# Kernel tuning notes

Hardware: AMD Instinct MI355X
Metric: run time of the kernel (lower is better)

Reference implementation:

```python
import jax, jax.numpy as jnp
import numpy as np

B, S, D, K, DF, H, DFF = 2, 512, 512, 8, 64, 8, 2048
DH = D // H  # d_head = 64
CS = D // K  # chunk_size = 64


def layer_norm(x, g, b, eps=1e-5):
    m = x.mean(-1, keepdims=True)
    v = ((x - m) ** 2).mean(-1, keepdims=True)
    return (x - m) / jnp.sqrt(v + eps) * g + b


def matexp_taylor(M, terms=6):
    # exp(M) ~= I + M + M^2/2! + ... (6 terms), batched over leading dims
    I = jnp.broadcast_to(jnp.eye(M.shape[-1], dtype=M.dtype), M.shape)
    res, P = I, I
    for n in range(1, terms + 1):
        P = jnp.matmul(P, M) / n
        res = res + P
    return res


def setup_inputs() -> dict:
    key = jax.random.key(0)
    ks = jax.random.split(key, 24)
    w = lambda k, shape, s=0.02: (jax.random.normal(k, shape, jnp.float32) * s)
    return {
        'x': jax.random.normal(ks[0], (B, S, D), jnp.float32),
        'u': jax.random.normal(ks[1], (B, S, DF), jnp.float32),
        'Wq': w(ks[2], (D, D)), 'bq': jnp.zeros((D,), jnp.float32),
        'Wk': w(ks[3], (D, D)), 'bk': jnp.zeros((D,), jnp.float32),
        'Wv': w(ks[4], (D, D)), 'bv': jnp.zeros((D,), jnp.float32),
        'Wo': w(ks[5], (D, D)), 'bo': jnp.zeros((D,), jnp.float32),
        'Wfp': w(ks[6], (DF, D)), 'bfp': jnp.zeros((D,), jnp.float32),
        'Wfo': w(ks[7], (D, DF)), 'bfo': jnp.zeros((DF,), jnp.float32),
        'Wc1': w(ks[8], (D, DFF)), 'bc1': jnp.zeros((DFF,), jnp.float32),
        'g_ln': jnp.ones((DFF,), jnp.float32), 'b_ln': jnp.zeros((DFF,), jnp.float32),
        # small scale keeps the Lie elements O(1) so the Taylor matexp is well-behaved
        'Wc2': w(ks[9], (DFF, D * K * K), 0.001), 'bc2': jnp.zeros((D * K * K,), jnp.float32),
    }


def reference(x, u, Wq, bq, Wk, bk, Wv, bv, Wo, bo, Wfp, bfp, Wfo, bfo,
              Wc1, bc1, g_ln, b_ln, Wc2, bc2):
    b, s, d = x.shape
    # --- ConnectionNetwork: A[b,s,d,k,k] ---
    h = jax.nn.gelu(x @ Wc1 + bc1, approximate=False)
    h = layer_norm(h, g_ln, b_ln)
    A = (h @ Wc2 + bc2).reshape(b, s, d, K, K)
    # --- ParallelTransport: lie[b,i,j] = sum_d (x_i - x_j)_d * A[j,d]  ---
    # (split into x_i.A_j and x_j.A_j terms to avoid [b,s,s,d,k,k] intermediate)
    lie = jnp.einsum('bid,bjdkl->bijkl', x, A) - jnp.einsum('bjd,bjdkl->bjkl', x, A)[:, None]
    Gamma = matexp_taylor(-lie)  # [b,s,s,k,k], Gamma[b,i,j] transports j->i
    # --- standard multi-head attention on x (eval mode, no dropout, no mask) ---
    q = (x @ Wq + bq).reshape(b, s, H, DH).transpose(0, 2, 1, 3)
    k_ = (x @ Wk + bk).reshape(b, s, H, DH).transpose(0, 2, 1, 3)
    v = (x @ Wv + bv).reshape(b, s, H, DH).transpose(0, 2, 1, 3)
    scores = jnp.einsum('bhid,bhjd->bhij', q, k_) / jnp.sqrt(jnp.float32(DH))
    attn = jax.nn.softmax(scores, axis=-1)
    ctx = jnp.einsum('bhij,bhjd->bhid', attn, v).transpose(0, 2, 1, 3).reshape(b, s, d)
    x_out = x + ctx @ Wo + bo
    # --- fiber transport: u_i += sum_j attn_avg[i,j] * Gamma[i,j] @ u_chunks[j] ---
    u_proj = u @ Wfp + bfp                      # [b,s,D]
    u_chunks = u_proj.reshape(b, s, K, CS)      # [b,s,k,cs]
    attn_avg = attn.mean(axis=1)                # [b,s,s]
    weighted = Gamma * attn_avg[..., None, None]
    u_t = jnp.einsum('bijkl,bjlc->bikc', weighted, u_chunks).reshape(b, s, d)
    u_out = u + u_t @ Wfo + bfo
    return (x_out, u_out)
```

## Files before the change

### kernel.cpp

```cpp
#include <hip/hip_runtime.h>
#include <math.h>

#define BB 2
#define SS 512
#define DD 512
#define HH 8
#define DFF 2048

typedef __attribute__((ext_vector_type(8))) short bf16x8;
typedef __attribute__((ext_vector_type(4))) float f32x4;

__device__ __forceinline__ float gelu_exact(float v) {
    return 0.5f * v * (1.0f + erff(v * 0.70710678118654752f));
}
__device__ __forceinline__ unsigned short f2bf(float f) {
    unsigned u = __float_as_uint(f);
    u += 0x7FFF + ((u >> 16) & 1);
    return (unsigned short)(u >> 16);
}
__device__ __forceinline__ float bf2f(unsigned short s) {
    return __uint_as_float(((unsigned)s) << 16);
}
__device__ __forceinline__ void gload16(const void* g, void* l) {
    __builtin_amdgcn_global_load_lds((const __attribute__((address_space(1))) void*)g,
                                     (__attribute__((address_space(3))) void*)l, 16, 0, 0);
}

template<int NT, int EPI, int SK = 1>
__global__ __launch_bounds__(256)
void mgemm_k(const unsigned short* __restrict__ A, const unsigned short* __restrict__ B,
             const float* __restrict__ bias, const float* __restrict__ resid,
             float* __restrict__ Cf, unsigned short* __restrict__ Cb,
             int K, int lda, int ldb, int ldc, int batchH,
             long aSB, long aSH, long bSB, long bSH, long cSB, long cSH,
             float scale)
{
    __shared__ unsigned short As[128][32];
    __shared__ unsigned short Bs[NT][32];
    const int tid = threadIdx.x;
    const int wave = tid >> 6, lane = tid & 63;
    const int z = blockIdx.z;
    const int zb = z / batchH, zh = z % batchH;
    const unsigned short* Ab = A + (long)zb * aSB + (long)zh * aSH;
    const unsigned short* Bb = B + (long)zb * bSB + (long)zh * bSH;
    const int chunk = (SK > 1) ? ((int)blockIdx.x % SK) : 0;
    const int colb  = (SK > 1) ? ((int)blockIdx.x / SK) : (int)blockIdx.x;
    const int row0 = blockIdx.y * 128, col0 = colb * NT;
    const int wm = wave >> 1, wn = wave & 1;
    const int lm = lane & 15, quad = lane >> 4;
    const int lrow = lane >> 2, lk = (lane & 3) * 8;
    constexpr int NTW = NT / 32;
    f32x4 acc[4][NTW];
    #pragma unroll
    for (int i = 0; i < 4; ++i)
        #pragma unroll
        for (int j = 0; j < NTW; ++j) acc[i][j] = (f32x4)0.f;

    const int kLo = chunk * (K / SK), kHi = kLo + K / SK;
    for (int k0 = kLo; k0 < kHi; k0 += 32) {
        #pragma unroll
        for (int t = 0; t < 2; ++t) {
            const int r = wave * 32 + t * 16;
            gload16(Ab + (long)(row0 + r + lrow) * lda + k0 + lk, &As[r][0]);
        }
        if (NT == 128) {
            #pragma unroll
            for (int t = 0; t < 2; ++t) {
                const int r = wave * 32 + t * 16;
                gload16(Bb + (long)(col0 + r + lrow) * ldb + k0 + lk, &Bs[r][0]);
            }
        } else {
            const int r = wave * 16;
            gload16(Bb + (long)(col0 + r + lrow) * ldb + k0 + lk, &Bs[r][0]);
        }
        __syncthreads();
        bf16x8 af[4], bfr[NTW];
        #pragma unroll
        for (int mt = 0; mt < 4; ++mt)
            af[mt] = *(const bf16x8*)&As[wm * 64 + mt * 16 + lm][quad * 8];
        #pragma unroll
        for (int nt = 0; nt < NTW; ++nt)
            bfr[nt] = *(const bf16x8*)&Bs[wn * (NT / 2) + nt * 16 + lm][quad * 8];
        #pragma unroll
        for (int mt = 0; mt < 4; ++mt)
            #pragma unroll
            for (int nt = 0; nt < NTW; ++nt)
                acc[mt][nt] = __builtin_amdgcn_mfma_f32_16x16x32_bf16(
                    af[mt], bfr[nt], acc[mt][nt], 0, 0, 0);
        __syncthreads();
    }
    float* Cfz = (Cf && EPI != 7) ? Cf + (long)zb * cSB + (long)zh * cSH : Cf;
    unsigned short* Cbz = Cb ? Cb + (long)zb * cSB + (long)zh * cSH : nullptr;
    #pragma unroll
    for (int mt = 0; mt < 4; ++mt) {
        #pragma unroll
        for (int nt = 0; nt < NTW; ++nt) {
            #pragma unroll
            for (int r = 0; r < 4; ++r) {
                const int row = row0 + wm * 64 + mt * 16 + quad * 4 + r;
                const int col = col0 + wn * (NT / 2) + nt * 16 + lm;
                float v = acc[mt][nt][r] * scale;
                if (EPI == 2)      v += bias[(col & 511) * 64 + (col >> 9)];
                else if (EPI == 1 || EPI == 4) v += bias[col];
                else if ((EPI == 3 || EPI == 5 || EPI == 6) && bias) v += bias[col];
                if (EPI == 1) v = gelu_exact(v);
                if (EPI == 4) v += resid[(long)row * ldc + col];
                if (EPI == 0 || EPI == 1 || EPI == 4)
                    Cfz[(long)row * ldc + col] = v;
                else if (EPI == 7)
                    Cf[(long)z * cSB + (long)chunk * cSH + (long)row * ldc + col] = v;
                else if (EPI == 2 || EPI == 3)
                    Cbz[(long)row * ldc + col] = f2bf(v);
                else if (EPI == 5)
                    Cb[(long)(row >> 9) * 262144 + (col >> 6) * 32768 +
                       (col & 63) * 512 + (row & 511)] = f2bf(v);
                else if (EPI == 6)
                    Cb[(long)(row >> 9) * 262144 + (col & 63) * 4096 +
                       (row & 511) * 8 + (col >> 6)] = f2bf(v);
            }
        }
    }
}

__global__ __launch_bounds__(256)
void redqk_k(const float* __restrict__ p, const float* __restrict__ bias,
             unsigned short* __restrict__ out)
{
    const long idx = (long)blockIdx.x * 256 + threadIdx.x;
    const float s = p[idx] + p[idx + 524288] + p[idx + 1048576] + p[idx + 1572864]
                  + bias[idx & 511];
    out[idx] = f2bf(s);
}
__global__ __launch_bounds__(256)
void redv_k(const float* __restrict__ p, const float* __restrict__ bias,
            unsigned short* __restrict__ vT)
{
    const long idx = (long)blockIdx.x * 256 + threadIdx.x;
    const int col = (int)(idx & 511);
    const float s = p[idx] + p[idx + 524288] + p[idx + 1048576] + p[idx + 1572864]
                  + bias[col];
    vT[(idx >> 18) * 262144 + (col >> 6) * 32768 + (col & 63) * 512 +
       ((idx >> 9) & 511)] = f2bf(s);
}
__global__ __launch_bounds__(256)
void redwo_k(const float* __restrict__ p, const float* __restrict__ bias,
             const float* __restrict__ resid, float* __restrict__ out)
{
    const long idx = (long)blockIdx.x * 256 + threadIdx.x;
    out[idx] = resid[idx] + bias[idx & 511]
             + p[idx] + p[idx + 524288] + p[idx + 1048576] + p[idx + 1572864];
}
template<int SK>
__global__ __launch_bounds__(256)
void redzc_k(const float* __restrict__ p, unsigned short* __restrict__ out)
{
    const long idx = (long)blockIdx.x * 256 + threadIdx.x;
    float s = 0.f;
    #pragma unroll
    for (int k = 0; k < SK; ++k) s += p[idx + (long)k * 524288];
    const int b = (int)(idx >> 18), zh = (int)((idx >> 15) & 7);
    const long rem = idx & 32767;
    const int i = (int)(rem >> 6), c = (int)(rem & 63);
    out[(long)b * 262144 + (long)i * 512 + zh * 64 + c] = f2bf(s);
}
__global__ __launch_bounds__(256)
void redu_k(const float* __restrict__ p, const float* __restrict__ bias,
            const float* __restrict__ resid, float* __restrict__ out)
{
    const long idx = (long)blockIdx.x * 256 + threadIdx.x;
    out[idx] = resid[idx] + bias[idx & 63]
             + p[idx] + p[idx + 65536] + p[idx + 131072] + p[idx + 196608];
}

__global__ __launch_bounds__(512, 2)
void fc2_k(const unsigned short* __restrict__ A, const unsigned short* __restrict__ Bm,
           const float* __restrict__ bias, unsigned short* __restrict__ C)
{
    extern __shared__ unsigned short smraw[];
#define SMA(ab, h) (smraw + (((ab) * 2 + (h)) * 8192))
#define SMB(bb, h) (smraw + (32768 + ((bb) * 2 + (h)) * 8192))
    const int tid = threadIdx.x;
    const int wave = tid >> 6, lane = tid & 63;
    const int bid = blockIdx.x;
    const int lin = (bid & 7) * 64 + (bid >> 3);
    const int by = lin & 3, bx = lin >> 2;
    const int row0 = by * 256, col0 = bx * 256;
    const int wm = wave >> 2, wn = wave & 3;
    const int lm = lane & 15, quad = lane >> 4;
    const int axor = lm & 7;
    const int arow = (wm * 64 + lm) * 64;
    const int brow = (wn * 32 + lm) * 64;
    const int ca0 = ((quad) ^ axor) * 8;
    const int ca1 = ((quad + 4) ^ axor) * 8;
    const int srow = wave * 8 + (lane >> 3);
    const int scx = ((lane & 7) ^ ((lane >> 3) & 7)) * 8;
    const int sbrow = ((srow >> 5) << 6) + (srow & 31);
    const unsigned short* AgB = A + (long)(row0 + srow) * 2048 + scx;
    const unsigned short* BgB = Bm + (long)(col0 + sbrow) * 2048 + scx;

    f32x4 acc[8][4];
    #pragma unroll
    for (int i = 0; i < 8; ++i)
        #pragma unroll
        for (int j = 0; j < 4; ++j) acc[i][j] = (f32x4)0.f;
    bf16x8 afr[4][2], b0f[2][2], b1f[2][2];

#define STGA(ab, h, toff) do { \
        const unsigned short* _g = AgB + (toff) * 64 + (h) * (64 * 2048); \
        unsigned short* _d = SMA(ab, h) + wave * 512; \
        gload16(_g, _d); \
        gload16(_g + 128 * 2048, _d + 4096); \
    } while (0)
#define STGB(bb, h, toff) do { \
        const unsigned short* _g = BgB + (toff) * 64 + (h) * (32 * 2048); \
        unsigned short* _d = SMB(bb, h) + wave * 512; \
        gload16(_g, _d); \
        gload16(_g + 128 * 2048, _d + 4096); \
    } while (0)
#define RDA(Hp) do { _Pragma("unroll") for (int _m = 0; _m < 4; ++_m) { \
        afr[_m][0] = *(const bf16x8*)((Hp) + arow + _m * 1024 + ca0); \
        afr[_m][1] = *(const bf16x8*)((Hp) + arow + _m * 1024 + ca1); } } while (0)
#define RDB(bf, Hp) do { _Pragma("unroll") for (int _n = 0; _n < 2; ++_n) { \
        bf[_n][0] = *(const bf16x8*)((Hp) + brow + _n * 1024 + ca0); \
        bf[_n][1] = *(const bf16x8*)((Hp) + brow + _n * 1024 + ca1); } } while (0)
#define MM(QM, QN, bf) do { _Pragma("unroll") for (int _m = 0; _m < 4; ++_m) \
        _Pragma("unroll") for (int _n = 0; _n < 2; ++_n) { \
        acc[(QM)*4+_m][(QN)*2+_n] = __builtin_amdgcn_mfma_f32_16x16x32_bf16( \
            afr[_m][0], bf[_n][0], acc[(QM)*4+_m][(QN)*2+_n], 0, 0, 0); \
        acc[(QM)*4+_m][(QN)*2+_n] = __builtin_amdgcn_mfma_f32_16x16x32_bf16( \
            afr[_m][1], bf[_n][1], acc[(QM)*4+_m][(QN)*2+_n], 0, 0, 0); } } while (0)
#define PH_MID() \
        __builtin_amdgcn_s_barrier(); \
        asm volatile("s_waitcnt lgkmcnt(0)" ::: "memory"); \
        __builtin_amdgcn_sched_barrier(0); \
        __builtin_amdgcn_s_setprio(1)
#define PH_END(VM) \
        __builtin_amdgcn_s_setprio(0); \
        __builtin_amdgcn_sched_barrier(0); \
        asm volatile("s_waitcnt vmcnt(" #VM ")" ::: "memory"); \
        __builtin_amdgcn_sched_barrier(0); \
        __builtin_amdgcn_s_barrier()
#define PH_END_NW() \
        __builtin_amdgcn_s_setprio(0); \
        __builtin_amdgcn_sched_barrier(0); \
        __builtin_amdgcn_s_barrier()

    STGB(0, 0, 0);
    STGB(0, 1, 0);
    STGA(0, 0, 0);
    STGA(0, 1, 0);
    STGB(1, 0, 1);
    STGB(1, 1, 1);
    asm volatile("s_waitcnt vmcnt(6)" ::: "memory");
    __builtin_amdgcn_s_barrier();

    int rA = 0;
    int rB = 0, mB = 1, wB = 2;
    #pragma unroll 1
    for (int t = 0; t < 32; ++t) {
        const int tA = (t + 1 < 32) ? (t + 1) : 31;
        const int tB = (t + 2 < 32) ? (t + 2) : 31;
        const unsigned short* A0p = SMA(rA, 0);
        const unsigned short* A1p = SMA(rA, 1);
        const unsigned short* B0p = SMB(rB, 0);
        const unsigned short* B1p = SMB(rB, 1);
        RDA(A0p); RDB(b0f, B0p);
        STGA(rA ^ 1, 0, tA);
        PH_MID(); MM(0, 0, b0f); PH_END_NW();
        RDB(b1f, B1p);
        STGA(rA ^ 1, 1, tA);
        PH_MID(); MM(0, 1, b1f); PH_END(8);
        RDA(A1p);
        STGB(wB, 0, tB);
        PH_MID(); MM(1, 1, b1f); PH_END_NW();
        STGB(wB, 1, tB);
        PH_MID(); MM(1, 0, b0f); PH_END(6);
        rA ^= 1;
        const int tmp = rB; rB = mB; mB = wB; wB = tmp;
    }
    asm volatile("s_waitcnt vmcnt(0)" ::: "memory");

    const int crow = row0 + wm * 128 + quad * 4;
    const int ccol0 = col0 + wn * 64 + lm;
    #pragma unroll
    for (int ms = 0; ms < 8; ++ms)
        #pragma unroll
        for (int ns = 0; ns < 4; ++ns) {
            const int col = ccol0 + ns * 16;
            const float bv = bias[(col & 511) * 64 + (col >> 9)];
            #pragma unroll
            for (int r = 0; r < 4; ++r) {
                const int row = crow + ms * 16 + r;
                C[(long)row * 32768 + col] = f2bf(acc[ms][ns][r] + bv);
            }
        }
#undef SMA
#undef SMB
#undef STGA
#undef STGB
#undef RDA
#undef RDB
#undef MM
#undef PH_MID
#undef PH_END
#undef PH_END_NW
}

__global__ __launch_bounds__(256)
void liegamma_k(const unsigned short* __restrict__ xb, const unsigned short* __restrict__ At,
                const float* __restrict__ xa, const float* __restrict__ aavg,
                unsigned short* __restrict__ Gw)
{
    __shared__ unsigned short Xs[128][32];
    __shared__ unsigned short Ts[64][32];
    __shared__ float Ml[128][68];
    const int tid = threadIdx.x;
    const int wave = tid >> 6, lane = tid & 63;
    const int b = blockIdx.z, j = blockIdx.y;
    const int i0 = blockIdx.x * 128;
    const int lm = lane & 15, quad = lane >> 4;
    const int lrow = lane >> 2, lk = (lane & 3) * 8;
    const unsigned short* Xb = xb + ((long)b * 512 + i0) * 512;
    const unsigned short* Tb = At + ((long)(b * 512 + j)) * 32768;
    f32x4 acc[2][4];
    #pragma unroll
    for (int i = 0; i < 2; ++i)
        #pragma unroll
        for (int n = 0; n < 4; ++n) acc[i][n] = (f32x4)0.f;

    for (int k0 = 0; k0 < 512; k0 += 32) {
        #pragma unroll
        for (int t = 0; t < 2; ++t) {
            const int r = wave * 32 + t * 16;
            gload16(Xb + (long)(r + lrow) * 512 + k0 + lk, &Xs[r][0]);
        }
        {
            const int r = wave * 16;
            gload16(Tb + (long)(r + lrow) * 512 + k0 + lk, &Ts[r][0]);
        }
        __syncthreads();
        bf16x8 af[2], bfr[4];
        #pragma unroll
        for (int mt = 0; mt < 2; ++mt)
            af[mt] = *(const bf16x8*)&Xs[wave * 32 + mt * 16 + lm][quad * 8];
        #pragma unroll
        for (int nt = 0; nt < 4; ++nt)
            bfr[nt] = *(const bf16x8*)&Ts[nt * 16 + lm][quad * 8];
        #pragma unroll
        for (int mt = 0; mt < 2; ++mt)
            #pragma unroll
            for (int nt = 0; nt < 4; ++nt)
                acc[mt][nt] = __builtin_amdgcn_mfma_f32_16x16x32_bf16(
                    af[mt], bfr[nt], acc[mt][nt], 0, 0, 0);
        __syncthreads();
    }
    const float* xar = xa + ((long)(b * 512 + j)) * 64;
    #pragma unroll
    for (int mt = 0; mt < 2; ++mt)
        #pragma unroll
        for (int nt = 0; nt < 4; ++nt) {
            const float xv = xar[nt * 16 + lm];
            #pragma unroll
            for (int r = 0; r < 4; ++r)
                Ml[wave * 32 + mt * 16 + quad * 4 + r][nt * 16 + lm] = xv - acc[mt][nt][r];
        }
    __syncthreads();
    const int r8 = tid & 7, mg = tid >> 3;
    #pragma unroll 1
    for (int pass = 0; pass < 4; ++pass) {
        const int mi = pass * 32 + mg;
        const f32x4* Mr = (const f32x4*)&Ml[mi][0];
        f32x4 Mreg[16];
        #pragma unroll
        for (int l = 0; l < 16; ++l) Mreg[l] = Mr[l];
        float P[8], res[8];
        #pragma unroll
        for (int c = 0; c < 8; ++c) { const float iv = (c == r8) ? 1.f : 0.f; P[c] = iv; res[c] = iv; }
        #pragma unroll
        for (int n = 1; n <= 6; ++n) {
            float tmp[8] = {0.f,0.f,0.f,0.f,0.f,0.f,0.f,0.f};
            const float invn = 1.f / (float)n;
            #pragma unroll
            for (int l = 0; l < 8; ++l) {
                const f32x4 m0 = Mreg[l * 2], m1 = Mreg[l * 2 + 1];
                const float pl = P[l];
                #pragma unroll
                for (int c = 0; c < 4; ++c) {
                    tmp[c]     = fmaf(pl, m0[c], tmp[c]);
                    tmp[4 + c] = fmaf(pl, m1[c], tmp[4 + c]);
                }
            }
            #pragma unroll
            for (int c = 0; c < 8; ++c) { P[c] = tmp[c] * invn; res[c] += P[c]; }
        }
        const float av = aavg[((long)b * 512 + i0 + mi) * 512 + j];
        bf16x8 o;
        #pragma unroll
        for (int c = 0; c < 8; ++c) o[c] = (short)f2bf(res[c] * av);
        *(bf16x8*)(Gw + ((long)(b * 8 + r8) * 512 + (i0 + mi)) * 4096 + (long)j * 8) = o;
    }
}

__global__ __launch_bounds__(256)
void lnbf_k(const float* __restrict__ h, const float* __restrict__ g,
            const float* __restrict__ b, unsigned short* __restrict__ out)
{
    const long row = blockIdx.x;
    const float* r = h + row * (long)DFF;
    const int tid = threadIdx.x;
    float vals[8];
    float s = 0.f, sq = 0.f;
    #pragma unroll
    for (int e = 0; e < 8; ++e) {
        const float v = r[tid + e * 256];
        vals[e] = v; s += v; sq += v * v;
    }
    __shared__ float rs[256], rq[256];
    rs[tid] = s; rq[tid] = sq; __syncthreads();
    for (int st = 128; st > 0; st >>= 1) {
        if (tid < st) { rs[tid] += rs[tid + st]; rq[tid] += rq[tid + st]; }
        __syncthreads();
    }
    const float mean = rs[0] * (1.f / DFF);
    const float var  = rq[0] * (1.f / DFF) - mean * mean;
    const float inv  = rsqrtf(var + 1e-5f);
    unsigned short* o = out + row * (long)DFF;
    #pragma unroll
    for (int e = 0; e < 8; ++e) {
        const int c = tid + e * 256;
        o[c] = f2bf((vals[e] - mean) * inv * g[c] + b[c]);
    }
}

__global__ __launch_bounds__(256)
void xa_k(const float* __restrict__ x, const unsigned short* __restrict__ At,
          float* __restrict__ xa)
{
    const int bj = blockIdx.x;
    const int tid = threadIdx.x;
    const int kl = tid >> 2, q = tid & 3;
    const unsigned short* Ar = At + (long)bj * 32768 + kl * 512 + q * 128;
    const float* xr = x + (long)bj * 512 + q * 128;
    float s = 0.f;
    #pragma unroll
    for (int d0 = 0; d0 < 128; d0 += 8) {
        const bf16x8 a = *(const bf16x8*)&Ar[d0];
        const f32x4 x0 = *(const f32x4*)&xr[d0];
        const f32x4 x1 = *(const f32x4*)&xr[d0 + 4];
        s = fmaf(x0[0], bf2f((unsigned short)a[0]), s);
        s = fmaf(x0[1], bf2f((unsigned short)a[1]), s);
        s = fmaf(x0[2], bf2f((unsigned short)a[2]), s);
        s = fmaf(x0[3], bf2f((unsigned short)a[3]), s);
        s = fmaf(x1[0], bf2f((unsigned short)a[4]), s);
        s = fmaf(x1[1], bf2f((unsigned short)a[5]), s);
        s = fmaf(x1[2], bf2f((unsigned short)a[6]), s);
        s = fmaf(x1[3], bf2f((unsigned short)a[7]), s);
    }
    __shared__ float red[64][5];
    red[kl][q] = s; __syncthreads();
    if (q == 0)
        xa[(long)bj * 64 + kl] = red[kl][0] + red[kl][1] + red[kl][2] + red[kl][3];
}

__global__ __launch_bounds__(256)
void softmax_k(float* __restrict__ p, unsigned short* __restrict__ pb)
{
    const long row = blockIdx.x;
    float* r = p + row * 512;
    const int tid = threadIdx.x;
    float v0 = r[tid], v1 = r[tid + 256];
    __shared__ float red[256];
    red[tid] = fmaxf(v0, v1); __syncthreads();
    for (int s = 128; s > 0; s >>= 1) {
        if (tid < s) red[tid] = fmaxf(red[tid], red[tid + s]);
        __syncthreads();
    }
    const float m = red[0]; __syncthreads();
    v0 = expf(v0 - m); v1 = expf(v1 - m);
    red[tid] = v0 + v1; __syncthreads();
    for (int s = 128; s > 0; s >>= 1) {
        if (tid < s) red[tid] += red[tid + s];
        __syncthreads();
    }
    const float inv = 1.f / red[0];
    const float a0 = v0 * inv, a1 = v1 * inv;
    r[tid] = a0; r[tid + 256] = a1;
    unsigned short* rb = pb + row * 512;
    rb[tid] = f2bf(a0); rb[tid + 256] = f2bf(a1);
}

__global__ __launch_bounds__(256)
void aavg_k(const float* __restrict__ attn, float* __restrict__ aavg)
{
    const long idx = (long)blockIdx.x * 256 + threadIdx.x;
    const int b = (int)(idx >> 18);
    const long rem = idx & 262143;
    float s = 0.f;
    #pragma unroll
    for (int h = 0; h < HH; ++h)
        s += attn[(long)b * 2097152 + (long)h * 262144 + rem];
    aavg[idx] = s * 0.125f;
}

__global__ __launch_bounds__(256)
void tconv_k(const float* __restrict__ in, unsigned short* __restrict__ out,
             int R, int C)
{
    __shared__ float Ls[64][65];
    const int c0 = blockIdx.x * 64, r0 = blockIdx.y * 64;
    const int tid = threadIdx.x;
    const int tc = tid & 63, tr = tid >> 6;
    #pragma unroll
    for (int p = 0; p < 16; ++p)
        Ls[tr + p * 4][tc] = in[(long)(r0 + tr + p * 4) * C + c0 + tc];
    __syncthreads();
    #pragma unroll
    for (int p = 0; p < 16; ++p)
        out[(long)(c0 + tr + p * 4) * R + r0 + tc] = f2bf(Ls[tc][tr + p * 4]);
}

__global__ __launch_bounds__(256)
void wc2p_k(const float* __restrict__ in, unsigned short* __restrict__ out)
{
    __shared__ float Ls[64][65];
    const int d0 = blockIdx.x;
    const long f0 = blockIdx.y * 64;
    const int tid = threadIdx.x;
    const int tc = tid & 63, tr = tid >> 6;
    #pragma unroll
    for (int p = 0; p < 16; ++p)
        Ls[tr + p * 4][tc] = in[(f0 + tr + p * 4) * 32768 + (long)d0 * 64 + tc];
    __syncthreads();
    #pragma unroll
    for (int p = 0; p < 16; ++p) {
        const int kl = tr + p * 4;
        out[((long)kl * 512 + d0) * 2048 + f0 + tc] = f2bf(Ls[tc][kl]);
    }
}

__global__ __launch_bounds__(256)
void f2bf_k(const float* __restrict__ in, unsigned short* __restrict__ out, int n)
{
    const int i = blockIdx.x * 256 + threadIdx.x;
    if (i < n) out[i] = f2bf(in[i]);
}

extern "C" void kernel_launch(void* const* d_in, const int* in_sizes, int n_in,
                              void* d_out, int out_size, void* d_ws, size_t ws_size,
                              hipStream_t stream) {
    const float* x   = (const float*)d_in[0];
    const float* u   = (const float*)d_in[1];
    const float* Wq  = (const float*)d_in[2];  const float* bq  = (const float*)d_in[3];
    const float* Wk  = (const float*)d_in[4];  const float* bk  = (const float*)d_in[5];
    const float* Wv  = (const float*)d_in[6];  const float* bv  = (const float*)d_in[7];
    const float* Wo  = (const float*)d_in[8];  const float* bo  = (const float*)d_in[9];
    const float* Wfp = (const float*)d_in[10]; const float* bfp = (const float*)d_in[11];
    const float* Wfo = (const float*)d_in[12]; const float* bfo = (const float*)d_in[13];
    const float* Wc1 = (const float*)d_in[14]; const float* bc1 = (const float*)d_in[15];
    const float* gln = (const float*)d_in[16]; const float* bln = (const float*)d_in[17];
    const float* Wc2 = (const float*)d_in[18]; const float* bc2 = (const float*)d_in[19];

    float* ws = (float*)d_ws;
    unsigned short* Wc2p = (unsigned short*)(ws);
    unsigned short* Gw   = (unsigned short*)(ws);
    unsigned short* At   = (unsigned short*)(ws + 33554432);
    float*          h    = ws + 50331648;
    unsigned short* h_bf = (unsigned short*)(ws + 52428800);
    unsigned short* x_bf = (unsigned short*)(ws + 53477376);
    unsigned short* u_bf = (unsigned short*)(ws + 53739520);
    unsigned short* Wc1t = (unsigned short*)(ws + 53772288);
    unsigned short* Wqt  = (unsigned short*)(ws + 54296576);
    unsigned short* Wkt  = (unsigned short*)(ws + 54427648);
    unsigned short* Wvt  = (unsigned short*)(ws + 54558720);
    unsigned short* Wot  = (unsigned short*)(ws + 54689792);
    unsigned short* Wfpt = (unsigned short*)(ws + 54820864);
    unsigned short* Wfot = (unsigned short*)(ws + 54837248);
    float*          xa   = ws + 54853632;
    unsigned short* q_bf = (unsigned short*)(ws + 54919168);
    unsigned short* k_bf = (unsigned short*)(ws + 55181312);
    unsigned short* vT   = (unsigned short*)(ws + 55443456);
    float*          sc   = ws + 55705600;
    unsigned short* at_bf= (unsigned short*)(ws + 59899904);
    float*          av   = ws + 61997056;
    unsigned short* ctx  = (unsigned short*)(ws + 62521344);
    unsigned short* upT2 = (unsigned short*)(ws + 62783488);
    unsigned short* ut_bf= (unsigned short*)(ws + 63045632);
    float*          qp   = ws + 63307776;
    float*          kp   = ws + 65404928;
    float*          vp   = ws + 67502080;
    float*          wop  = ws + 69599232;
    float*          ctxp = ws + 71696384;
    float*          utp  = ws + 73793536;
    float*          up   = ws + 77987840;
    float* xout = (float*)d_out;
    float* uout = xout + 524288;

    const dim3 blk(256);

    hipFuncSetAttribute(reinterpret_cast<const void*>(fc2_k),
                        hipFuncAttributeMaxDynamicSharedMemorySize, 163840);

    tconv_k<<<dim3(32, 8), blk, 0, stream>>>(Wc1, Wc1t, 512, 2048);
    tconv_k<<<dim3(8, 8), blk, 0, stream>>>(Wq, Wqt, 512, 512);
    tconv_k<<<dim3(8, 8), blk, 0, stream>>>(Wk, Wkt, 512, 512);
    tconv_k<<<dim3(8, 8), blk, 0, stream>>>(Wv, Wvt, 512, 512);
    tconv_k<<<dim3(8, 8), blk, 0, stream>>>(Wo, Wot, 512, 512);
    tconv_k<<<dim3(8, 1), blk, 0, stream>>>(Wfp, Wfpt, 64, 512);
    tconv_k<<<dim3(1, 8), blk, 0, stream>>>(Wfo, Wfot, 512, 64);
    wc2p_k<<<dim3(512, 32), blk, 0, stream>>>(Wc2, Wc2p);
    f2bf_k<<<dim3(2048), blk, 0, stream>>>(x, x_bf, 524288);
    f2bf_k<<<dim3(256), blk, 0, stream>>>(u, u_bf, 65536);

    mgemm_k<128,7,4><<<dim3(16, 8, 1), blk, 0, stream>>>(
        x_bf, Wqt, nullptr, nullptr, qp, nullptr, 512, 512, 512, 512,
        1, 0,0,0,0, 0,524288, 1.0f);
    redqk_k<<<dim3(2048), blk, 0, stream>>>(qp, bq, q_bf);
    mgemm_k<128,7,4><<<dim3(16, 8, 1), blk, 0, stream>>>(
        x_bf, Wkt, nullptr, nullptr, kp, nullptr, 512, 512, 512, 512,
        1, 0,0,0,0, 0,524288, 1.0f);
    redqk_k<<<dim3(2048), blk, 0, stream>>>(kp, bk, k_bf);
    mgemm_k<128,7,4><<<dim3(16, 8, 1), blk, 0, stream>>>(
        x_bf, Wvt, nullptr, nullptr, vp, nullptr, 512, 512, 512, 512,
        1, 0,0,0,0, 0,524288, 1.0f);
    redv_k<<<dim3(2048), blk, 0, stream>>>(vp, bv, vT);
    mgemm_k<128,0><<<dim3(4, 4, 16), blk, 0, stream>>>(
        q_bf, k_bf, nullptr, nullptr, sc, nullptr, 64, 512, 512, 512,
        8, 262144,64, 262144,64, 2097152,262144, 0.125f);
    softmax_k<<<dim3(BB * HH * SS), blk, 0, stream>>>(sc, at_bf);
    aavg_k<<<dim3(2048), blk, 0, stream>>>(sc, av);
    mgemm_k<64,7,4><<<dim3(4, 4, 16), blk, 0, stream>>>(
        at_bf, vT, nullptr, nullptr, ctxp, nullptr, 512, 512, 512, 64,
        8, 2097152,262144, 262144,32768, 32768,524288, 1.0f);
    redzc_k<4><<<dim3(2048), blk, 0, stream>>>(ctxp, ctx);
    mgemm_k<128,7,4><<<dim3(16, 8, 1), blk, 0, stream>>>(
        ctx, Wot, nullptr, nullptr, wop, nullptr, 512, 512, 512, 512,
        1, 0,0,0,0, 0,524288, 1.0f);
    redwo_k<<<dim3(2048), blk, 0, stream>>>(wop, bo, x, xout);

    mgemm_k<128,1><<<dim3(16, 8, 1), blk, 0, stream>>>(
        x_bf, Wc1t, bc1, nullptr, h, nullptr, 512, 512, 512, 2048,
        1, 0,0,0,0,0,0, 1.0f);
    lnbf_k<<<dim3(1024), blk, 0, stream>>>(h, gln, bln, h_bf);
    fc2_k<<<dim3(512), dim3(512), 163840, stream>>>(h_bf, Wc2p, bc2, At);
    xa_k<<<dim3(1024), blk, 0, stream>>>(x, At, xa);
    liegamma_k<<<dim3(4, 512, 2), blk, 0, stream>>>(x_bf, At, xa, av, Gw);

    mgemm_k<128,6><<<dim3(4, 8, 1), blk, 0, stream>>>(
        u_bf, Wfpt, bfp, nullptr, nullptr, upT2, 64, 64, 64, 512,
        1, 0,0,0,0,0,0, 1.0f);
    mgemm_k<64,7,8><<<dim3(8, 4, 16), blk, 0, stream>>>(
        Gw, upT2, nullptr, nullptr, utp, nullptr, 4096, 4096, 4096, 64,
        8, 16777216,2097152, 262144,0, 32768,524288, 1.0f);
    redzc_k<8><<<dim3(2048), blk, 0, stream>>>(utp, ut_bf);
    mgemm_k<64,7,4><<<dim3(4, 8, 1), blk, 0, stream>>>(
        ut_bf, Wfot, nullptr, nullptr, up, nullptr, 512, 512, 512, 64,
        1, 0,0,0,0, 0,65536, 1.0f);
    redu_k<<<dim3(256), blk, 0, stream>>>(up, bfo, u, uout);
}
```

Measured before the change: 866.1 us.

## Fuse QKV projections into one GEMM, fold xa into liegamma, batch transposes

Concatenates the Q/K/V weight transposes so one split-K GEMM with N=1536 replaces three GEMMs, and one combined reduction kernel replaces the three per-projection reductions. The xa dot product (x_j · A_j) is now computed inside liegamma_k from the A tile already staged in shared memory, which removes the separate xa_k kernel. The four 512x512 weight transposes become one batched launch. The goal is fewer launches and no second read of At. The catch is that each liegamma block (4 per j) now recomputes xa redundantly and uses more shared memory.

```diff
diff --git a/kernel.cpp b/kernel.cpp
--- a/kernel.cpp
+++ b/kernel.cpp
@@ -123,24 +123,26 @@
 }
 
 __global__ __launch_bounds__(256)
-void redqk_k(const float* __restrict__ p, const float* __restrict__ bias,
-             unsigned short* __restrict__ out)
-{
-    const long idx = (long)blockIdx.x * 256 + threadIdx.x;
-    const float s = p[idx] + p[idx + 524288] + p[idx + 1048576] + p[idx + 1572864]
-                  + bias[idx & 511];
-    out[idx] = f2bf(s);
-}
-__global__ __launch_bounds__(256)
-void redv_k(const float* __restrict__ p, const float* __restrict__ bias,
-            unsigned short* __restrict__ vT)
-{
-    const long idx = (long)blockIdx.x * 256 + threadIdx.x;
-    const int col = (int)(idx & 511);
-    const float s = p[idx] + p[idx + 524288] + p[idx + 1048576] + p[idx + 1572864]
-                  + bias[col];
-    vT[(idx >> 18) * 262144 + (col >> 6) * 32768 + (col & 63) * 512 +
-       ((idx >> 9) & 511)] = f2bf(s);
+void redqkv_k(const float* __restrict__ p, const float* __restrict__ bq,
+              const float* __restrict__ bk, const float* __restrict__ bv,
+              unsigned short* __restrict__ q_bf, unsigned short* __restrict__ k_bf,
+              unsigned short* __restrict__ vT)
+{
+    const int col = blockIdx.x * 256 + threadIdx.x;
+    const int row = blockIdx.y;
+    const long base = (long)row * 1536 + col;
+    float s = p[base] + p[base + 1572864] + p[base + 3145728] + p[base + 4718592];
+    const int which = col >> 9;
+    const int scol = col & 511;
+    if (which == 0) {
+        q_bf[(long)row * 512 + scol] = f2bf(s + bq[scol]);
+    } else if (which == 1) {
+        k_bf[(long)row * 512 + scol] = f2bf(s + bk[scol]);
+    } else {
+        s += bv[scol];
+        vT[(long)(row >> 9) * 262144 + (scol >> 6) * 32768 +
+           (scol & 63) * 512 + (row & 511)] = f2bf(s);
+    }
 }
 __global__ __launch_bounds__(256)
 void redwo_k(const float* __restrict__ p, const float* __restrict__ bias,
@@ -308,12 +310,15 @@
 
 __global__ __launch_bounds__(256)
 void liegamma_k(const unsigned short* __restrict__ xb, const unsigned short* __restrict__ At,
-                const float* __restrict__ xa, const float* __restrict__ aavg,
+                const float* __restrict__ xf, const float* __restrict__ aavg,
                 unsigned short* __restrict__ Gw)
 {
     __shared__ unsigned short Xs[128][32];
     __shared__ unsigned short Ts[64][32];
     __shared__ float Ml[128][68];
+    __shared__ float xjs[512];
+    __shared__ float xred[64][4];
+    __shared__ float xafin[64];
     const int tid = threadIdx.x;
     const int wave = tid >> 6, lane = tid & 63;
     const int b = blockIdx.z, j = blockIdx.y;
@@ -322,11 +327,16 @@
     const int lrow = lane >> 2, lk = (lane & 3) * 8;
     const unsigned short* Xb = xb + ((long)b * 512 + i0) * 512;
     const unsigned short* Tb = At + ((long)(b * 512 + j)) * 32768;
+    const float* xrow = xf + ((long)b * 512 + j) * 512;
+    xjs[tid] = xrow[tid];
+    xjs[tid + 256] = xrow[tid + 256];
     f32x4 acc[2][4];
     #pragma unroll
     for (int i = 0; i < 2; ++i)
         #pragma unroll
         for (int n = 0; n < 4; ++n) acc[i][n] = (f32x4)0.f;
+    float xas = 0.f;
+    const int kl2 = tid >> 2, q2 = tid & 3;
 
     for (int k0 = 0; k0 < 512; k0 += 32) {
         #pragma unroll
@@ -352,14 +362,25 @@
             for (int nt = 0; nt < 4; ++nt)
                 acc[mt][nt] = __builtin_amdgcn_mfma_f32_16x16x32_bf16(
                     af[mt], bfr[nt], acc[mt][nt], 0, 0, 0);
+        {
+            const bf16x8 tv = *(const bf16x8*)&Ts[kl2][q2 * 8];
+            const float* xs = &xjs[k0 + q2 * 8];
+            #pragma unroll
+            for (int e = 0; e < 8; ++e)
+                xas = fmaf(xs[e], bf2f((unsigned short)tv[e]), xas);
+        }
         __syncthreads();
     }
-    const float* xar = xa + ((long)(b * 512 + j)) * 64;
+    xred[kl2][q2] = xas;
+    __syncthreads();
+    if (tid < 64)
+        xafin[tid] = xred[tid][0] + xred[tid][1] + xred[tid][2] + xred[tid][3];
+    __syncthreads();
     #pragma unroll
     for (int mt = 0; mt < 2; ++mt)
         #pragma unroll
         for (int nt = 0; nt < 4; ++nt) {
-            const float xv = xar[nt * 16 + lm];
+            const float xv = xafin[nt * 16 + lm];
             #pragma unroll
             for (int r = 0; r < 4; ++r)
                 Ml[wave * 32 + mt * 16 + quad * 4 + r][nt * 16 + lm] = xv - acc[mt][nt][r];
@@ -433,36 +454,6 @@
 }
 
 __global__ __launch_bounds__(256)
-void xa_k(const float* __restrict__ x, const unsigned short* __restrict__ At,
-          float* __restrict__ xa)
-{
-    const int bj = blockIdx.x;
-    const int tid = threadIdx.x;
-    const int kl = tid >> 2, q = tid & 3;
-    const unsigned short* Ar = At + (long)bj * 32768 + kl * 512 + q * 128;
-    const float* xr = x + (long)bj * 512 + q * 128;
-    float s = 0.f;
-    #pragma unroll
-    for (int d0 = 0; d0 < 128; d0 += 8) {
-        const bf16x8 a = *(const bf16x8*)&Ar[d0];
-        const f32x4 x0 = *(const f32x4*)&xr[d0];
-        const f32x4 x1 = *(const f32x4*)&xr[d0 + 4];
-        s = fmaf(x0[0], bf2f((unsigned short)a[0]), s);
-        s = fmaf(x0[1], bf2f((unsigned short)a[1]), s);
-        s = fmaf(x0[2], bf2f((unsigned short)a[2]), s);
-        s = fmaf(x0[3], bf2f((unsigned short)a[3]), s);
-        s = fmaf(x1[0], bf2f((unsigned short)a[4]), s);
-        s = fmaf(x1[1], bf2f((unsigned short)a[5]), s);
-        s = fmaf(x1[2], bf2f((unsigned short)a[6]), s);
-        s = fmaf(x1[3], bf2f((unsigned short)a[7]), s);
-    }
-    __shared__ float red[64][5];
-    red[kl][q] = s; __syncthreads();
-    if (q == 0)
-        xa[(long)bj * 64 + kl] = red[kl][0] + red[kl][1] + red[kl][2] + red[kl][3];
-}
-
-__global__ __launch_bounds__(256)
 void softmax_k(float* __restrict__ p, unsigned short* __restrict__ pb)
 {
     const long row = blockIdx.x;
@@ -517,6 +508,27 @@
     #pragma unroll
     for (int p = 0; p < 16; ++p)
         out[(long)(c0 + tr + p * 4) * R + r0 + tc] = f2bf(Ls[tc][tr + p * 4]);
+}
+
+__global__ __launch_bounds__(256)
+void tconv4_k(const float* __restrict__ W0, const float* __restrict__ W1,
+              const float* __restrict__ W2, const float* __restrict__ W3,
+              unsigned short* __restrict__ outbase)
+{
+    __shared__ float Ls[64][65];
+    const int z = blockIdx.z;
+    const float* in = (z == 0) ? W0 : (z == 1) ? W1 : (z == 2) ? W2 : W3;
+    unsigned short* out = outbase + (long)z * 262144;
+    const int c0 = blockIdx.x * 64, r0 = blockIdx.y * 64;
+    const int tid = threadIdx.x;
+    const int tc = tid & 63, tr = tid >> 6;
+    #pragma unroll
+    for (int p = 0; p < 16; ++p)
+        Ls[tr + p * 4][tc] = in[(long)(r0 + tr + p * 4) * 512 + c0 + tc];
+    __syncthreads();
+    #pragma unroll
+    for (int p = 0; p < 16; ++p)
+        out[(long)(c0 + tr + p * 4) * 512 + r0 + tc] = f2bf(Ls[tc][tr + p * 4]);
 }
 
 __global__ __launch_bounds__(256)
@@ -585,15 +597,14 @@
     unsigned short* ctx  = (unsigned short*)(ws + 62521344);
     unsigned short* upT2 = (unsigned short*)(ws + 62783488);
     unsigned short* ut_bf= (unsigned short*)(ws + 63045632);
-    float*          qp   = ws + 63307776;
-    float*          kp   = ws + 65404928;
-    float*          vp   = ws + 67502080;
+    float*          qkvp = ws + 63307776;
     float*          wop  = ws + 69599232;
     float*          ctxp = ws + 71696384;
     float*          utp  = ws + 73793536;
     float*          up   = ws + 77987840;
     float* xout = (float*)d_out;
     float* uout = xout + 524288;
+    (void)xa;
 
     const dim3 blk(256);
 
@@ -601,28 +612,17 @@
                         hipFuncAttributeMaxDynamicSharedMemorySize, 163840);
 
     tconv_k<<<dim3(32, 8), blk, 0, stream>>>(Wc1, Wc1t, 512, 2048);
-    tconv_k<<<dim3(8, 8), blk, 0, stream>>>(Wq, Wqt, 512, 512);
-    tconv_k<<<dim3(8, 8), blk, 0, stream>>>(Wk, Wkt, 512, 512);
-    tconv_k<<<dim3(8, 8), blk, 0, stream>>>(Wv, Wvt, 512, 512);
-    tconv_k<<<dim3(8, 8), blk, 0, stream>>>(Wo, Wot, 512, 512);
+    tconv4_k<<<dim3(8, 8, 4), blk, 0, stream>>>(Wq, Wk, Wv, Wo, Wqt);
     tconv_k<<<dim3(8, 1), blk, 0, stream>>>(Wfp, Wfpt, 64, 512);
     tconv_k<<<dim3(1, 8), blk, 0, stream>>>(Wfo, Wfot, 512, 64);
     wc2p_k<<<dim3(512, 32), blk, 0, stream>>>(Wc2, Wc2p);
     f2bf_k<<<dim3(2048), blk, 0, stream>>>(x, x_bf, 524288);
     f2bf_k<<<dim3(256), blk, 0, stream>>>(u, u_bf, 65536);
 
-    mgemm_k<128,7,4><<<dim3(16, 8, 1), blk, 0, stream>>>(
-        x_bf, Wqt, nullptr, nullptr, qp, nullptr, 512, 512, 512, 512,
-        1, 0,0,0,0, 0,524288, 1.0f);
-    redqk_k<<<dim3(2048), blk, 0, stream>>>(qp, bq, q_bf);
-    mgemm_k<128,7,4><<<dim3(16, 8, 1), blk, 0, stream>>>(
-        x_bf, Wkt, nullptr, nullptr, kp, nullptr, 512, 512, 512, 512,
-        1, 0,0,0,0, 0,524288, 1.0f);
-    redqk_k<<<dim3(2048), blk, 0, stream>>>(kp, bk, k_bf);
-    mgemm_k<128,7,4><<<dim3(16, 8, 1), blk, 0, stream>>>(
-        x_bf, Wvt, nullptr, nullptr, vp, nullptr, 512, 512, 512, 512,
-        1, 0,0,0,0, 0,524288, 1.0f);
-    redv_k<<<dim3(2048), blk, 0, stream>>>(vp, bv, vT);
+    mgemm_k<128,7,4><<<dim3(48, 8, 1), blk, 0, stream>>>(
+        x_bf, Wqt, nullptr, nullptr, qkvp, nullptr, 512, 512, 512, 1536,
+        1, 0,0,0,0, 0,1572864, 1.0f);
+    redqkv_k<<<dim3(6, 1024), blk, 0, stream>>>(qkvp, bq, bk, bv, q_bf, k_bf, vT);
     mgemm_k<128,0><<<dim3(4, 4, 16), blk, 0, stream>>>(
         q_bf, k_bf, nullptr, nullptr, sc, nullptr, 64, 512, 512, 512,
         8, 262144,64, 262144,64, 2097152,262144, 0.125f);
@@ -642,8 +642,7 @@
         1, 0,0,0,0,0,0, 1.0f);
     lnbf_k<<<dim3(1024), blk, 0, stream>>>(h, gln, bln, h_bf);
     fc2_k<<<dim3(512), dim3(512), 163840, stream>>>(h_bf, Wc2p, bc2, At);
-    xa_k<<<dim3(1024), blk, 0, stream>>>(x, At, xa);
-    liegamma_k<<<dim3(4, 512, 2), blk, 0, stream>>>(x_bf, At, xa, av, Gw);
+    liegamma_k<<<dim3(4, 512, 2), blk, 0, stream>>>(x_bf, At, x, av, Gw);
 
     mgemm_k<128,6><<<dim3(4, 8, 1), blk, 0, stream>>>(
         u_bf, Wfpt, bfp, nullptr, nullptr, upT2, 64, 64, 64, 512,
```

Result: faster. 822.9 us (-5.0%).
